# Kernel tuning notes

Hardware: AMD Instinct MI355X
Metric: run time of the kernel (lower is better)

## Reference

```python
import jax, jax.numpy as jnp
import numpy as np

V = 512      # vq_num_vocabs
T = 128      # code_dim
H = 512      # plug_hidden_dim
L = 2        # plug_num_layers
B = 512      # batch


def setup_inputs() -> dict:
    key = jax.random.key(0)
    ks = jax.random.split(key, 12)
    s = 1.0 / np.sqrt(H)
    x = jax.random.randint(ks[0], (B, T), 0, V)
    y = jax.random.normal(ks[1], (B,), jnp.float32)
    emb = jax.random.normal(ks[2], (V + 1, H), jnp.float32) * 0.02
    yW = jax.random.uniform(ks[3], (H, 1), jnp.float32, -1.0, 1.0)
    yb = jax.random.uniform(ks[4], (H,), jnp.float32, -1.0, 1.0)
    Wih = jax.random.uniform(ks[5], (L, 4 * H, H), jnp.float32, -s, s)
    Whh = jax.random.uniform(ks[6], (L, 4 * H, H), jnp.float32, -s, s)
    bih = jax.random.uniform(ks[7], (L, 4 * H), jnp.float32, -s, s)
    bhh = jax.random.uniform(ks[8], (L, 4 * H), jnp.float32, -s, s)
    decW = jax.random.uniform(ks[9], (V, H), jnp.float32, -s, s)
    decb = jax.random.uniform(ks[10], (V,), jnp.float32, -s, s)
    return dict(x=x, y=y, emb=emb, yW=yW, yb=yb, Wih=Wih, Whh=Whh,
                bih=bih, bhh=bhh, decW=decW, decb=decb)


def _lstm(inp, Wih, Whh, bih, bhh):
    # inp: [B, T, H]; PyTorch gate order i, f, g, o
    out = inp
    for l in range(Wih.shape[0]):
        Wi, Wh, bi, bh = Wih[l], Whh[l], bih[l], bhh[l]
        xg = jnp.einsum('bth,gh->btg', out, Wi) + bi + bh  # [B, T, 4H]

        def step(carry, xg_t):
            h, c = carry
            g = xg_t + h @ Wh.T
            i, f, gg, o = jnp.split(g, 4, axis=-1)
            c = jax.nn.sigmoid(f) * c + jax.nn.sigmoid(i) * jnp.tanh(gg)
            h = jax.nn.sigmoid(o) * jnp.tanh(c)
            return (h, c), h

        h0 = jnp.zeros((out.shape[0], Wh.shape[1]), out.dtype)
        _, hs = jax.lax.scan(step, (h0, h0), jnp.swapaxes(xg, 0, 1))
        out = jnp.swapaxes(hs, 0, 1)  # [B, T, H]
    return out


def reference(x, y, emb, yW, yb, Wih, Whh, bih, bhh, decW, decb):
    # teacher_forcing_ratio = 1.0 (deterministic): input at step t is
    # start token at t=0, then x[:, t-1].
    start = jnp.full((x.shape[0], 1), V, x.dtype)
    trg = jnp.concatenate([start, x[:, :-1]], axis=1)      # [B, T]
    y_enc = y[:, None] @ yW.T + yb                          # [B, H]
    inp = emb[trg] + y_enc[:, None, :]                      # [B, T, H]
    h = _lstm(inp, Wih, Whh, bih, bhh)                      # [B, T, H]
    logits = jnp.einsum('bth,vh->btv', h, decW) + decb      # [B, T, V]
    return logits
```

## Files before the change

kernel.cpp:

```cpp
#include <hip/hip_runtime.h>
#include <hip/hip_bf16.h>
#include <string.h>

typedef __bf16 bf16;
typedef __bf16 bf16x8 __attribute__((ext_vector_type(8)));
typedef __bf16 bf16x4 __attribute__((ext_vector_type(4)));
typedef __bf16 bf16x2 __attribute__((ext_vector_type(2)));
typedef float f32x4 __attribute__((ext_vector_type(4)));
typedef float f32x2 __attribute__((ext_vector_type(2)));
typedef unsigned long long ull;

__global__ void convert_w(const float* __restrict__ Wih, const float* __restrict__ Whh,
                          const float* __restrict__ decW, const float* __restrict__ bih,
                          const float* __restrict__ bhh,
                          bf16* __restrict__ WihB, bf16* __restrict__ WhhB,
                          bf16* __restrict__ decWB, float* __restrict__ bias) {
    int idx = blockIdx.x * 256 + threadIdx.x;
    const int NW = 2 * 2048 * 512;
    if (idx < NW) {
        WihB[idx] = (bf16)Wih[idx];
    } else if (idx < 2 * NW) {
        WhhB[idx - NW] = (bf16)Whh[idx - NW];
    } else if (idx < 2 * NW + 512 * 512) {
        decWB[idx - 2 * NW] = (bf16)decW[idx - 2 * NW];
    } else if (idx < 2 * NW + 512 * 512 + 4096) {
        int j = idx - (2 * NW + 512 * 512);
        bias[j] = bih[j] + bhh[j];
    }
}

__global__ void prep_inp(const int* __restrict__ x, const float* __restrict__ y,
                         const float* __restrict__ emb, const float* __restrict__ yW,
                         const float* __restrict__ yb, bf16* __restrict__ inp) {
    int idx = blockIdx.x * 256 + threadIdx.x;
    int bt = idx >> 6;
    int h0 = (idx & 63) * 8;
    int b = bt >> 7, t = bt & 127;
    int trg = (t == 0) ? 512 : x[b * 128 + t - 1];
    float yv = y[b];
    const float* e = emb + (size_t)trg * 512 + h0;
    bf16x8 v;
    #pragma unroll
    for (int i = 0; i < 8; ++i) v[i] = (bf16)(e[i] + yv * yW[h0 + i] + yb[h0 + i]);
    *(bf16x8*)&inp[(size_t)bt * 512 + h0] = v;
}

template <bool OUT_BF16>
__global__ __launch_bounds__(256) void gemm_bt(const bf16* __restrict__ A,
                                               const bf16* __restrict__ W,
                                               const float* __restrict__ bias,
                                               void* __restrict__ Cout, int M, int N) {
    constexpr int K = 512;
    __shared__ bf16 As[128][40];
    __shared__ bf16 Ws[128][40];
    int bid = blockIdx.x;
    int nTiles = N / 128;
    int m0 = (bid / nTiles) * 128;
    int n0 = (bid % nTiles) * 128;
    int tid = threadIdx.x;
    int wave = tid >> 6, lane = tid & 63;
    int quad = lane >> 4, l16 = lane & 15;
    int wm = (wave & 1) * 64, wn = (wave >> 1) * 64;
    f32x4 acc[4][4] = {};

    for (int k0 = 0; k0 < K; k0 += 32) {
        __syncthreads();
        #pragma unroll
        for (int r = 0; r < 2; ++r) {
            int c = tid + 256 * r;
            int row = c >> 2, col = (c & 3) * 8;
            *(bf16x8*)&As[row][col] = *(const bf16x8*)&A[(size_t)(m0 + row) * K + k0 + col];
            *(bf16x8*)&Ws[row][col] = *(const bf16x8*)&W[(size_t)(n0 + row) * K + k0 + col];
        }
        __syncthreads();
        bf16x8 af[4], bfr[4];
        #pragma unroll
        for (int i = 0; i < 4; ++i) af[i] = *(const bf16x8*)&As[wm + i * 16 + l16][quad * 8];
        #pragma unroll
        for (int i = 0; i < 4; ++i) bfr[i] = *(const bf16x8*)&Ws[wn + i * 16 + l16][quad * 8];
        #pragma unroll
        for (int mt = 0; mt < 4; ++mt)
            #pragma unroll
            for (int nt = 0; nt < 4; ++nt)
                acc[mt][nt] = __builtin_amdgcn_mfma_f32_16x16x32_bf16(af[mt], bfr[nt], acc[mt][nt], 0, 0, 0);
    }

    #pragma unroll
    for (int mt = 0; mt < 4; ++mt)
        #pragma unroll
        for (int nt = 0; nt < 4; ++nt) {
            int row = m0 + wm + mt * 16 + quad * 4;
            int col = n0 + wn + nt * 16 + l16;
            float bv = bias[col];
            #pragma unroll
            for (int i = 0; i < 4; ++i) {
                float v = acc[mt][nt][i] + bv;
                if (OUT_BF16) ((bf16*)Cout)[(size_t)(row + i) * N + col] = (bf16)v;
                else          ((float*)Cout)[(size_t)(row + i) * N + col] = v;
            }
        }
}

#define GROUP 8
#define HS_STRIDE 520

__global__ __launch_bounds__(512, 2) void lstm_scan(const bf16* __restrict__ xg,
                                                    const bf16* __restrict__ Wh,
                                                    bf16* __restrict__ hA,
                                                    bf16* __restrict__ hB,
                                                    bf16* __restrict__ h_all,
                                                    unsigned* __restrict__ barcnt) {
    constexpr int T = 128;
    __shared__ bf16 Hs[16][HS_STRIDE];
    __shared__ float gs[8][16][36];
    int tid = threadIdx.x;
    int bt = blockIdx.x >> 3;
    int q  = blockIdx.x & 7;
    int b0 = bt * 16;
    int n0 = q * 64;
    int w = tid >> 6, lane = tid & 63;
    int quad = lane >> 4, l16 = lane & 15;
    int g = w >> 1, s = w & 1;
    unsigned* cnt = barcnt + bt * 64;

    bf16x8 wreg[2][16];
    const bf16* wbase = Wh + ((size_t)g * 512 + n0 + 32 * s) * 512;
    #pragma unroll
    for (int nt = 0; nt < 2; ++nt)
        #pragma unroll
        for (int kc = 0; kc < 16; ++kc)
            wreg[nt][kc] = *(const bf16x8*)&wbase[(size_t)(nt * 16 + l16) * 512 + kc * 32 + quad * 8];

    int m = tid >> 5;
    int nl0 = (tid & 31) * 2;
    int b = b0 + m;
    int half = nl0 >> 5;
    int nn = nl0 & 31;
    float cc[2] = {0.f, 0.f};

    __hip_atomic_store((unsigned*)&hA[(size_t)b * 512 + n0 + nl0], 0u,
                       __ATOMIC_RELAXED, __HIP_MEMORY_SCOPE_AGENT);
    asm volatile("s_waitcnt vmcnt(0)" ::: "memory");
    __syncthreads();
    if (tid == 0) __hip_atomic_store(cnt + q, 1u, __ATOMIC_RELAXED, __HIP_MEMORY_SCOPE_AGENT);

    const bf16* hp = hA;
    bf16* hn = hB;

    for (int t = 0; t < T; ++t) {
        size_t xrow = ((size_t)b * T + t) * 2048 + n0 + nl0;
        bf16x2 xv[4];
        #pragma unroll
        for (int gg = 0; gg < 4; ++gg) xv[gg] = *(const bf16x2*)&xg[xrow + (size_t)gg * 512];

        if (tid == 0) {
            unsigned tgt = (unsigned)(t + 1);
            for (;;) {
                unsigned mn = 0xffffffffu;
                #pragma unroll
                for (int i = 0; i < 8; ++i) {
                    unsigned v = __hip_atomic_load(cnt + i, __ATOMIC_RELAXED,
                                                   __HIP_MEMORY_SCOPE_AGENT);
                    mn = mn < v ? mn : v;
                }
                if (mn >= tgt) break;
                __builtin_amdgcn_s_sleep(1);
            }
        }
        __syncthreads();

        #pragma unroll
        for (int i = 0; i < 4; ++i) {
            int idx = i * 512 + tid;
            int row = idx >> 7, colb = idx & 127;
            ull v = __hip_atomic_load((const ull*)&hp[(size_t)(b0 + row) * 512 + colb * 4],
                                      __ATOMIC_RELAXED, __HIP_MEMORY_SCOPE_AGENT);
            *(ull*)&Hs[row][colb * 4] = v;
        }
        __syncthreads();

        f32x4 acc0 = {}, acc1 = {};
        #pragma unroll
        for (int kc = 0; kc < 16; ++kc) {
            bf16x8 af0 = *(const bf16x8*)&Hs[l16][kc * 32 + quad * 8];
            acc0 = __builtin_amdgcn_mfma_f32_16x16x32_bf16(af0, wreg[0][kc], acc0, 0, 0, 0);
            acc1 = __builtin_amdgcn_mfma_f32_16x16x32_bf16(af0, wreg[1][kc], acc1, 0, 0, 0);
        }
        #pragma unroll
        for (int i = 0; i < 4; ++i) {
            gs[w][quad * 4 + i][0 * 16 + l16] = acc0[i];
            gs[w][quad * 4 + i][1 * 16 + l16] = acc1[i];
        }
        __syncthreads();

        f32x2 g0 = *(const f32x2*)&gs[0 * 2 + half][m][nn];
        f32x2 g1 = *(const f32x2*)&gs[1 * 2 + half][m][nn];
        f32x2 g2 = *(const f32x2*)&gs[2 * 2 + half][m][nn];
        f32x2 g3 = *(const f32x2*)&gs[3 * 2 + half][m][nn];
        bf16x2 hv;
        #pragma unroll
        for (int ii = 0; ii < 2; ++ii) {
            float gi = g0[ii] + (float)xv[0][ii];
            float gf = g1[ii] + (float)xv[1][ii];
            float gg = g2[ii] + (float)xv[2][ii];
            float go = g3[ii] + (float)xv[3][ii];
            float iv = 1.f / (1.f + __expf(-gi));
            float fv = 1.f / (1.f + __expf(-gf));
            float gv = 1.f - 2.f / (1.f + __expf(2.f * gg));
            float ov = 1.f / (1.f + __expf(-go));
            float cn = fv * cc[ii] + iv * gv;
            float th = 1.f - 2.f / (1.f + __expf(2.f * cn));
            cc[ii] = cn;
            hv[ii] = (bf16)(ov * th);
        }
        unsigned hbits;
        memcpy(&hbits, &hv, 4);
        __hip_atomic_store((unsigned*)&hn[(size_t)b * 512 + n0 + nl0], hbits,
                           __ATOMIC_RELAXED, __HIP_MEMORY_SCOPE_AGENT);
        asm volatile("s_waitcnt vmcnt(0)" ::: "memory");
        __syncthreads();
        if (tid == 0) __hip_atomic_store(cnt + q, (unsigned)(t + 2),
                                         __ATOMIC_RELAXED, __HIP_MEMORY_SCOPE_AGENT);
        *(bf16x2*)&h_all[((size_t)b * T + t) * 512 + n0 + nl0] = hv;

        const bf16* tmp = hp; hp = hn; hn = (bf16*)tmp;
    }
}

extern "C" void kernel_launch(void* const* d_in, const int* in_sizes, int n_in,
                              void* d_out, int out_size, void* d_ws, size_t ws_size,
                              hipStream_t stream) {
    const int*   x    = (const int*)d_in[0];
    const float* y    = (const float*)d_in[1];
    const float* emb  = (const float*)d_in[2];
    const float* yW   = (const float*)d_in[3];
    const float* yb   = (const float*)d_in[4];
    const float* Wih  = (const float*)d_in[5];
    const float* Whh  = (const float*)d_in[6];
    const float* bih  = (const float*)d_in[7];
    const float* bhh  = (const float*)d_in[8];
    const float* decW = (const float*)d_in[9];
    const float* decb = (const float*)d_in[10];
    float* out = (float*)d_out;

    char* ws = (char*)d_ws;
    size_t off = 0;
    auto alloc = [&](size_t bytes) {
        char* p = ws + off;
        off += (bytes + 255) & ~(size_t)255;
        return p;
    };
    bf16*  inp   = (bf16*)alloc(65536ull * 512 * 2);
    bf16*  xg    = (bf16*)alloc(65536ull * 2048 * 2);
    bf16*  WihB  = (bf16*)alloc(2097152ull * 2);
    bf16*  WhhB  = (bf16*)alloc(2097152ull * 2);
    bf16*  decWB = (bf16*)alloc(262144ull * 2);
    float* bias  = (float*)alloc(4096ull * 4);
    bf16*  hA    = (bf16*)alloc(512ull * 512 * 2);
    bf16*  hB    = (bf16*)alloc(512ull * 512 * 2);
    unsigned* cnt = (unsigned*)alloc(2 * 32 * 64 * 4);

    hipMemsetAsync(cnt, 0, 2 * 32 * 64 * 4, stream);
    convert_w<<<17424, 256, 0, stream>>>(Wih, Whh, decW, bih, bhh, WihB, WhhB, decWB, bias);
    prep_inp<<<16384, 256, 0, stream>>>(x, y, emb, yW, yb, inp);

    const size_t LSTRIDE = 2048ull * 512;
    for (int l = 0; l < 2; ++l) {
        gemm_bt<true><<<512 * 16, 256, 0, stream>>>(inp, WihB + (size_t)l * LSTRIDE,
                                                    bias + l * 2048, xg, 65536, 2048);
        lstm_scan<<<256, 512, 0, stream>>>(xg, WhhB + (size_t)l * LSTRIDE,
                                           hA, hB, inp, cnt + (size_t)l * 32 * 64);
    }
    gemm_bt<false><<<512 * 4, 256, 0, stream>>>(inp, decWB, decb, out, 65536, 512);
}
```

Before: 1.675 ms.

## Split LSTM scan hidden dimension across 16 blocks per batch tile

The recurrent LSTM scan now splits each 16-row batch tile across 16 workgroups of 32 hidden units each instead of 8 of 64. This doubles the grid to 512 blocks and halves per-thread register weights and MFMA work per step, with launch bounds raised to allow more resident blocks. The aim is to shorten the per-timestep critical path by spreading the serial recurrence over more CUs. In exchange, each group barrier now polls 16 counters, h stores shrink to 2-byte atomics, and every block still reloads the full h tile each step.

Result: slower. 1.760 ms (+5.1%).

```diff
diff --git a/kernel.cpp b/kernel.cpp
--- a/kernel.cpp
+++ b/kernel.cpp
@@ -7,7 +7,6 @@
 typedef __bf16 bf16x4 __attribute__((ext_vector_type(4)));
 typedef __bf16 bf16x2 __attribute__((ext_vector_type(2)));
 typedef float f32x4 __attribute__((ext_vector_type(4)));
-typedef float f32x2 __attribute__((ext_vector_type(2)));
 typedef unsigned long long ull;
 
 __global__ void convert_w(const float* __restrict__ Wih, const float* __restrict__ Whh,
@@ -101,10 +100,9 @@
         }
 }
 
-#define GROUP 8
 #define HS_STRIDE 520
 
-__global__ __launch_bounds__(512, 2) void lstm_scan(const bf16* __restrict__ xg,
+__global__ __launch_bounds__(512, 4) void lstm_scan(const bf16* __restrict__ xg,
                                                     const bf16* __restrict__ Wh,
                                                     bf16* __restrict__ hA,
                                                     bf16* __restrict__ hB,
@@ -112,34 +110,37 @@
                                                     unsigned* __restrict__ barcnt) {
     constexpr int T = 128;
     __shared__ bf16 Hs[16][HS_STRIDE];
-    __shared__ float gs[8][16][36];
+    __shared__ float gs[8][16][17];
     int tid = threadIdx.x;
-    int bt = blockIdx.x >> 3;
-    int q  = blockIdx.x & 7;
+    int bt = blockIdx.x >> 4;
+    int q  = blockIdx.x & 15;
     int b0 = bt * 16;
-    int n0 = q * 64;
+    int n0 = q * 32;
     int w = tid >> 6, lane = tid & 63;
     int quad = lane >> 4, l16 = lane & 15;
     int g = w >> 1, s = w & 1;
     unsigned* cnt = barcnt + bt * 64;
 
-    bf16x8 wreg[2][16];
-    const bf16* wbase = Wh + ((size_t)g * 512 + n0 + 32 * s) * 512;
-    #pragma unroll
-    for (int nt = 0; nt < 2; ++nt)
-        #pragma unroll
-        for (int kc = 0; kc < 16; ++kc)
-            wreg[nt][kc] = *(const bf16x8*)&wbase[(size_t)(nt * 16 + l16) * 512 + kc * 32 + quad * 8];
+    bf16x8 wreg[16];
+    const bf16* wbase = Wh + ((size_t)(g * 512 + n0 + 16 * s)) * 512;
+    #pragma unroll
+    for (int kc = 0; kc < 16; ++kc)
+        wreg[kc] = *(const bf16x8*)&wbase[(size_t)l16 * 512 + kc * 32 + quad * 8];
 
     int m = tid >> 5;
-    int nl0 = (tid & 31) * 2;
+    int nl = tid & 31;
     int b = b0 + m;
-    int half = nl0 >> 5;
-    int nn = nl0 & 31;
-    float cc[2] = {0.f, 0.f};
-
-    __hip_atomic_store((unsigned*)&hA[(size_t)b * 512 + n0 + nl0], 0u,
-                       __ATOMIC_RELAXED, __HIP_MEMORY_SCOPE_AGENT);
+    int shalf = nl >> 4;
+    int nn = nl & 15;
+    float cc = 0.f;
+
+    #pragma unroll
+    for (int i = 0; i < 4; ++i) {
+        int idx = i * 512 + tid;
+        int row = idx >> 7, colb = idx & 127;
+        __hip_atomic_store((ull*)&hA[(size_t)(b0 + row) * 512 + colb * 4], 0ull,
+                           __ATOMIC_RELAXED, __HIP_MEMORY_SCOPE_AGENT);
+    }
     asm volatile("s_waitcnt vmcnt(0)" ::: "memory");
     __syncthreads();
     if (tid == 0) __hip_atomic_store(cnt + q, 1u, __ATOMIC_RELAXED, __HIP_MEMORY_SCOPE_AGENT);
@@ -148,23 +149,23 @@
     bf16* hn = hB;
 
     for (int t = 0; t < T; ++t) {
-        size_t xrow = ((size_t)b * T + t) * 2048 + n0 + nl0;
-        bf16x2 xv[4];
-        #pragma unroll
-        for (int gg = 0; gg < 4; ++gg) xv[gg] = *(const bf16x2*)&xg[xrow + (size_t)gg * 512];
+        size_t xrow = ((size_t)b * T + t) * 2048 + n0 + nl;
+        bf16 xv[4];
+        #pragma unroll
+        for (int gg = 0; gg < 4; ++gg) xv[gg] = xg[xrow + (size_t)gg * 512];
 
         if (tid == 0) {
             unsigned tgt = (unsigned)(t + 1);
             for (;;) {
                 unsigned mn = 0xffffffffu;
                 #pragma unroll
-                for (int i = 0; i < 8; ++i) {
+                for (int i = 0; i < 16; ++i) {
                     unsigned v = __hip_atomic_load(cnt + i, __ATOMIC_RELAXED,
                                                    __HIP_MEMORY_SCOPE_AGENT);
                     mn = mn < v ? mn : v;
                 }
                 if (mn >= tgt) break;
-                __builtin_amdgcn_s_sleep(1);
+                __builtin_amdgcn_s_sleep(2);
             }
         }
         __syncthreads();
@@ -179,49 +180,39 @@
         }
         __syncthreads();
 
-        f32x4 acc0 = {}, acc1 = {};
+        f32x4 acc = {};
         #pragma unroll
         for (int kc = 0; kc < 16; ++kc) {
-            bf16x8 af0 = *(const bf16x8*)&Hs[l16][kc * 32 + quad * 8];
-            acc0 = __builtin_amdgcn_mfma_f32_16x16x32_bf16(af0, wreg[0][kc], acc0, 0, 0, 0);
-            acc1 = __builtin_amdgcn_mfma_f32_16x16x32_bf16(af0, wreg[1][kc], acc1, 0, 0, 0);
-        }
-        #pragma unroll
-        for (int i = 0; i < 4; ++i) {
-            gs[w][quad * 4 + i][0 * 16 + l16] = acc0[i];
-            gs[w][quad * 4 + i][1 * 16 + l16] = acc1[i];
-        }
-        __syncthreads();
-
-        f32x2 g0 = *(const f32x2*)&gs[0 * 2 + half][m][nn];
-        f32x2 g1 = *(const f32x2*)&gs[1 * 2 + half][m][nn];
-        f32x2 g2 = *(const f32x2*)&gs[2 * 2 + half][m][nn];
-        f32x2 g3 = *(const f32x2*)&gs[3 * 2 + half][m][nn];
-        bf16x2 hv;
-        #pragma unroll
-        for (int ii = 0; ii < 2; ++ii) {
-            float gi = g0[ii] + (float)xv[0][ii];
-            float gf = g1[ii] + (float)xv[1][ii];
-            float gg = g2[ii] + (float)xv[2][ii];
-            float go = g3[ii] + (float)xv[3][ii];
-            float iv = 1.f / (1.f + __expf(-gi));
-            float fv = 1.f / (1.f + __expf(-gf));
-            float gv = 1.f - 2.f / (1.f + __expf(2.f * gg));
-            float ov = 1.f / (1.f + __expf(-go));
-            float cn = fv * cc[ii] + iv * gv;
-            float th = 1.f - 2.f / (1.f + __expf(2.f * cn));
-            cc[ii] = cn;
-            hv[ii] = (bf16)(ov * th);
-        }
-        unsigned hbits;
-        memcpy(&hbits, &hv, 4);
-        __hip_atomic_store((unsigned*)&hn[(size_t)b * 512 + n0 + nl0], hbits,
+            bf16x8 af = *(const bf16x8*)&Hs[l16][kc * 32 + quad * 8];
+            acc = __builtin_amdgcn_mfma_f32_16x16x32_bf16(af, wreg[kc], acc, 0, 0, 0);
+        }
+        #pragma unroll
+        for (int i = 0; i < 4; ++i)
+            gs[w][quad * 4 + i][l16] = acc[i];
+        __syncthreads();
+
+        float gi = gs[0 * 2 + shalf][m][nn] + (float)xv[0];
+        float gf = gs[1 * 2 + shalf][m][nn] + (float)xv[1];
+        float gg = gs[2 * 2 + shalf][m][nn] + (float)xv[2];
+        float go = gs[3 * 2 + shalf][m][nn] + (float)xv[3];
+        float iv = 1.f / (1.f + __expf(-gi));
+        float fv = 1.f / (1.f + __expf(-gf));
+        float gv = 1.f - 2.f / (1.f + __expf(2.f * gg));
+        float ov = 1.f / (1.f + __expf(-go));
+        float cn = fv * cc + iv * gv;
+        float th = 1.f - 2.f / (1.f + __expf(2.f * cn));
+        cc = cn;
+        bf16 hv = (bf16)(ov * th);
+
+        unsigned short hbits;
+        memcpy(&hbits, &hv, 2);
+        __hip_atomic_store((unsigned short*)&hn[(size_t)b * 512 + n0 + nl], hbits,
                            __ATOMIC_RELAXED, __HIP_MEMORY_SCOPE_AGENT);
         asm volatile("s_waitcnt vmcnt(0)" ::: "memory");
         __syncthreads();
         if (tid == 0) __hip_atomic_store(cnt + q, (unsigned)(t + 2),
                                          __ATOMIC_RELAXED, __HIP_MEMORY_SCOPE_AGENT);
-        *(bf16x2*)&h_all[((size_t)b * T + t) * 512 + n0 + nl0] = hv;
+        h_all[((size_t)b * T + t) * 512 + n0 + nl] = hv;
 
         const bf16* tmp = hp; hp = hn; hn = (bf16*)tmp;
     }
@@ -268,7 +259,7 @@
     for (int l = 0; l < 2; ++l) {
         gemm_bt<true><<<512 * 16, 256, 0, stream>>>(inp, WihB + (size_t)l * LSTRIDE,
                                                     bias + l * 2048, xg, 65536, 2048);
-        lstm_scan<<<256, 512, 0, stream>>>(xg, WhhB + (size_t)l * LSTRIDE,
+        lstm_scan<<<512, 512, 0, stream>>>(xg, WhhB + (size_t)l * LSTRIDE,
                                            hA, hB, inp, cnt + (size_t)l * 32 * 64);
     }
     gemm_bt<false><<<512 * 4, 256, 0, stream>>>(inp, decWB, decb, out, 65536, 512);
```
